# Kernel optimization log

Hardware: AMD Instinct MI355X
Metric: run time of the kernel (lower is better)

## Reference

```python
import jax, jax.numpy as jnp
import numpy as np


def setup_inputs() -> dict:
    key = jax.random.key(0)
    B, S, D, H = 4, 2048, 1024, 16
    hd = D // H
    ks = jax.random.split(key, 11)
    sc = 1.0 / np.sqrt(D)
    return {
        "keys": jax.random.normal(ks[0], (B, S, D), jnp.float32),
        "queries": jax.random.normal(ks[1], (B, S, D), jnp.float32),
        "values": jax.random.normal(ks[2], (B, S, D), jnp.float32),
        "Wq": jax.random.normal(ks[3], (H, D, hd), jnp.float32) * sc,
        "bq": jax.random.normal(ks[4], (H, hd), jnp.float32) * 0.02,
        "Wk": jax.random.normal(ks[5], (H, D, hd), jnp.float32) * sc,
        "bk": jax.random.normal(ks[6], (H, hd), jnp.float32) * 0.02,
        "Wv": jax.random.normal(ks[7], (H, D, hd), jnp.float32) * sc,
        "bv": jax.random.normal(ks[8], (H, hd), jnp.float32) * 0.02,
        "Wo": jax.random.normal(ks[9], (D, D), jnp.float32) * sc,
        "bo": jax.random.normal(ks[10], (D,), jnp.float32) * 0.02,
    }


def reference(keys, queries, values, Wq, bq, Wk, bk, Wv, bv, Wo, bo):
    # Per-head linear projections: [B,S,D] x [H,D,hd] -> [B,H,S,hd]
    q = jnp.einsum("bsd,hde->bhse", queries, Wq) + bq[None, :, None, :]
    k = jnp.einsum("bsd,hde->bhse", keys, Wk) + bk[None, :, None, :]
    v = jnp.einsum("bsd,hde->bhse", values, Wv) + bv[None, :, None, :]

    hd = q.shape[-1]
    S = q.shape[2]
    scores = jnp.einsum("bhse,bhte->bhst", q, k) / jnp.sqrt(jnp.float32(hd))
    causal = jnp.tril(jnp.ones((S, S), dtype=bool))  # tril buffer
    scores = jnp.where(causal[None, None, :, :], scores, -jnp.inf)
    attn = jax.nn.softmax(scores, axis=-1)  # dropout p=0 (eval)

    o = jnp.einsum("bhst,bhte->bhse", attn, v)  # [B,H,S,hd]
    # concat heads -> [B,S,H*hd]
    o = o.transpose(0, 2, 1, 3).reshape(o.shape[0], S, -1)
    return o @ Wo + bo
```

## Files before the change

### kernel.cpp

```cpp
#include <hip/hip_runtime.h>
#include <stdint.h>

typedef unsigned short u16;
typedef __attribute__((ext_vector_type(4))) float f32x4;
typedef __attribute__((ext_vector_type(8))) short bfrag;

static __device__ __forceinline__ u16 f2bf(float f) {
  union { float f; uint32_t u; } v; v.f = f;
  return (u16)((v.u + 0x7fffu + ((v.u >> 16) & 1u)) >> 16);
}
static __device__ __forceinline__ uint32_t cvtpk(float lo, float hi) {
  uint32_t r;
  asm("v_cvt_pk_bf16_f32 %0, %1, %2" : "=v"(r) : "v"(lo), "v"(hi));
  return r;
}
static __device__ __forceinline__ uint32_t pk2bf(float lo, float hi) {
  union { float f; uint32_t u; } a, b; a.f = lo; b.f = hi;
  return __builtin_amdgcn_perm(b.u + 0x8000u, a.u + 0x8000u, 0x07060302u);
}
static __device__ __forceinline__ float fexp2(float x) {
  float r;
  asm("v_exp_f32 %0, %1" : "=v"(r) : "v"(x));
  return r;
}

#define GLOAD16(gp, lp)                                              \
  __builtin_amdgcn_global_load_lds(                                  \
      (const __attribute__((address_space(1))) uint32_t*)(gp),       \
      (__attribute__((address_space(3))) uint32_t*)(lp), 16, 0, 0)

__global__ __launch_bounds__(256) void pack_w_hde(const float* __restrict__ W,
                                                  u16* __restrict__ Wt) {
  __shared__ float tile[64][65];
  const int h = blockIdx.y, k0 = blockIdx.x * 64;
  const int tid = threadIdx.x;
#pragma unroll
  for (int j = 0; j < 4; ++j) {
    int idx = tid + j * 256;
    int rr = idx >> 4, c4 = (idx & 15) * 4;
    const float4 v = *(const float4*)(W + (size_t)h * 65536 + (size_t)(k0 + rr) * 64 + c4);
    tile[rr][c4 + 0] = v.x; tile[rr][c4 + 1] = v.y;
    tile[rr][c4 + 2] = v.z; tile[rr][c4 + 3] = v.w;
  }
  __syncthreads();
#pragma unroll
  for (int j = 0; j < 4; ++j) {
    int idx = tid + j * 256;
    int ee = idx >> 4, c4 = (idx & 15) * 4;
    uint2 u;
    u.x = f2bf(tile[c4 + 0][ee]) | ((uint32_t)f2bf(tile[c4 + 1][ee]) << 16);
    u.y = f2bf(tile[c4 + 2][ee]) | ((uint32_t)f2bf(tile[c4 + 3][ee]) << 16);
    *(uint2*)(Wt + (size_t)(h * 64 + ee) * 1024 + k0 + c4) = u;
  }
}

__global__ __launch_bounds__(256) void transpose_w(const float* __restrict__ W,
                                                   u16* __restrict__ Wt) {
  __shared__ float tile[64][65];
  const int k0 = blockIdx.x * 64, n0 = blockIdx.y * 64;
  const int tid = threadIdx.x;
#pragma unroll
  for (int j = 0; j < 4; ++j) {
    int idx = tid + j * 256;
    int rr = idx >> 4, c4 = (idx & 15) * 4;
    const float4 v = *(const float4*)(W + (size_t)(k0 + rr) * 1024 + n0 + c4);
    tile[rr][c4 + 0] = v.x; tile[rr][c4 + 1] = v.y;
    tile[rr][c4 + 2] = v.z; tile[rr][c4 + 3] = v.w;
  }
  __syncthreads();
#pragma unroll
  for (int j = 0; j < 4; ++j) {
    int idx = tid + j * 256;
    int ee = idx >> 4, c4 = (idx & 15) * 4;
    uint2 u;
    u.x = f2bf(tile[c4 + 0][ee]) | ((uint32_t)f2bf(tile[c4 + 1][ee]) << 16);
    u.y = f2bf(tile[c4 + 2][ee]) | ((uint32_t)f2bf(tile[c4 + 3][ee]) << 16);
    *(uint2*)(Wt + (size_t)(n0 + ee) * 1024 + k0 + c4) = u;
  }
}

__global__ __launch_bounds__(256) void gemm_qkv(
    const float* __restrict__ Aq, const float* __restrict__ Ak,
    const float* __restrict__ Avv, const u16* __restrict__ Bt,
    const float* __restrict__ bq, const float* __restrict__ bk,
    const float* __restrict__ bv,
    u16* __restrict__ Qb, u16* __restrict__ Kb, u16* __restrict__ Vt) {
  __shared__ u16 As[2][128 * 32];
  __shared__ u16 Bs[2][128 * 32];
  const int tid = threadIdx.x;
  const int n = blockIdx.x;
  const int xcd = n & 7, j = n >> 3;
  const int mb = xcd * 8 + (j & 7);
  const int nb = j >> 3;
  const int chunk = nb >> 3;
  const float* Af = (chunk == 0) ? Aq : (chunk == 1) ? Ak : Avv;
  const int wid = tid >> 6, lane = tid & 63;
  const int wr = wid >> 1, wc = wid & 1;
  const int g = lane >> 4, l15 = lane & 15;
  f32x4 acc[4][4] = {};

  const int bsrc = ((lane & 3) ^ ((lane >> 3) & 3)) * 8;
  const u16* Bg = Bt + (size_t)(nb * 128 + 2 * wid * 16 + (lane >> 2)) * 1024 + bsrc;
  const float* Ap = Af + (size_t)(mb * 128 + (tid >> 2)) * 1024 + (tid & 3) * 8;
  const int arow = tid >> 2;
  const int acs = (((tid & 3) ^ ((tid >> 3) & 3))) * 8;
  const int swzr = (l15 >> 1) & 3;

  float4 fa[2][2];
#pragma unroll
  for (int c = 0; c < 2; ++c) {
    fa[c][0] = *(const float4*)(Ap + (size_t)c * 64 * 1024);
    fa[c][1] = *(const float4*)(Ap + (size_t)c * 64 * 1024 + 4);
  }
#pragma unroll
  for (int c = 0; c < 2; ++c)
    GLOAD16(Bg + (size_t)c * 16 * 1024, &Bs[0][2 * wid * 512 + c * 512]);
#pragma unroll
  for (int c = 0; c < 2; ++c) {
    uint4 u;
    u.x = pk2bf(fa[c][0].x, fa[c][0].y); u.y = pk2bf(fa[c][0].z, fa[c][0].w);
    u.z = pk2bf(fa[c][1].x, fa[c][1].y); u.w = pk2bf(fa[c][1].z, fa[c][1].w);
    *(uint4*)&As[0][(arow + c * 64) * 32 + acs] = u;
  }
  __syncthreads();
  int cur = 0;
  for (int kk = 0; kk < 32; ++kk) {
    if (kk < 31) {
      const int kn = (kk + 1) * 32;
#pragma unroll
      for (int c = 0; c < 2; ++c) {
        fa[c][0] = *(const float4*)(Ap + (size_t)c * 64 * 1024 + kn);
        fa[c][1] = *(const float4*)(Ap + (size_t)c * 64 * 1024 + kn + 4);
      }
#pragma unroll
      for (int c = 0; c < 2; ++c)
        GLOAD16(Bg + (size_t)c * 16 * 1024 + kn, &Bs[cur ^ 1][2 * wid * 512 + c * 512]);
    }
    bfrag a[4], b[4];
#pragma unroll
    for (int m = 0; m < 4; ++m)
      a[m] = __builtin_bit_cast(bfrag,
          *(const uint4*)&As[cur][(wr * 64 + m * 16 + l15) * 32 + ((g ^ swzr)) * 8]);
#pragma unroll
    for (int nn = 0; nn < 4; ++nn)
      b[nn] = __builtin_bit_cast(bfrag,
          *(const uint4*)&Bs[cur][(wc * 64 + nn * 16 + l15) * 32 + ((g ^ swzr)) * 8]);
    __builtin_amdgcn_s_setprio(1);
#pragma unroll
    for (int m = 0; m < 4; ++m)
#pragma unroll
      for (int nn = 0; nn < 4; ++nn)
        acc[m][nn] = __builtin_amdgcn_mfma_f32_16x16x32_bf16(a[m], b[nn], acc[m][nn], 0, 0, 0);
    __builtin_amdgcn_s_setprio(0);
    if (kk < 31) {
#pragma unroll
      for (int c = 0; c < 2; ++c) {
        uint4 u;
        u.x = pk2bf(fa[c][0].x, fa[c][0].y); u.y = pk2bf(fa[c][0].z, fa[c][0].w);
        u.z = pk2bf(fa[c][1].x, fa[c][1].y); u.w = pk2bf(fa[c][1].z, fa[c][1].w);
        *(uint4*)&As[cur ^ 1][(arow + c * 64) * 32 + acs] = u;
      }
      __syncthreads();
      cur ^= 1;
    }
  }

  const int row0 = mb * 128 + wr * 64 + g * 4;
  const int cc0 = (nb & 7) * 128 + wc * 64 + l15;
  const float* bias = (chunk == 0) ? bq : (chunk == 1) ? bk : bv;
  const float qs = (chunk == 0) ? 0.125f * 1.44269504f : 1.0f;
#pragma unroll
  for (int m = 0; m < 4; ++m) {
#pragma unroll
    for (int nn = 0; nn < 4; ++nn) {
      const int row = row0 + m * 16;
      const int cc = cc0 + nn * 16;
      const float bcv = bias[cc];
      if (chunk < 2) {
        u16* dst = (chunk == 0) ? Qb : Kb;
#pragma unroll
        for (int r = 0; r < 4; ++r)
          dst[(size_t)(row + r) * 1024 + cc] = f2bf((acc[m][nn][r] + bcv) * qs);
      } else {
        u16 w[4];
#pragma unroll
        for (int r = 0; r < 4; ++r) w[r] = f2bf(acc[m][nn][r] + bcv);
        const size_t dst =
            ((size_t)((row >> 11) * 16 + (cc >> 6)) * 64 + (cc & 63)) * 2048 + (row & 2047);
        *(uint2*)(Vt + dst) = *(const uint2*)w;
      }
    }
  }
}

__global__ __launch_bounds__(256) void gemm_o(const u16* __restrict__ Abf,
                                              const u16* __restrict__ Bt,
                                              const float* __restrict__ bo,
                                              float* __restrict__ Of) {
  __shared__ u16 As[2][128 * 32];
  __shared__ u16 Bs[2][128 * 32];
  const int tid = threadIdx.x;
  const int n = blockIdx.x;
  const int xcd = n & 7, j = n >> 3;
  const int mb = xcd * 8 + (j & 7);
  const int nb = j >> 3;
  const int wid = tid >> 6, lane = tid & 63;
  const int wr = wid >> 1, wc = wid & 1;
  const int g = lane >> 4, l15 = lane & 15;
  f32x4 acc[4][4] = {};

  const int bsrc = ((lane & 3) ^ ((lane >> 3) & 3)) * 8;
  const int swzr = (l15 >> 1) & 3;
  const u16* Bg = Bt + (size_t)(nb * 128 + 2 * wid * 16 + (lane >> 2)) * 1024 + bsrc;
  const u16* Ag = Abf + (size_t)(mb * 128 + 2 * wid * 16 + (lane >> 2)) * 1024 + bsrc;

#pragma unroll
  for (int c = 0; c < 2; ++c) {
    GLOAD16(Ag + (size_t)c * 16 * 1024, &As[0][2 * wid * 512 + c * 512]);
    GLOAD16(Bg + (size_t)c * 16 * 1024, &Bs[0][2 * wid * 512 + c * 512]);
  }
  __syncthreads();
  int cur = 0;
  for (int kk = 0; kk < 32; ++kk) {
    if (kk < 31) {
      const int kn = (kk + 1) * 32;
#pragma unroll
      for (int c = 0; c < 2; ++c) {
        GLOAD16(Ag + (size_t)c * 16 * 1024 + kn, &As[cur ^ 1][2 * wid * 512 + c * 512]);
        GLOAD16(Bg + (size_t)c * 16 * 1024 + kn, &Bs[cur ^ 1][2 * wid * 512 + c * 512]);
      }
    }
    bfrag a[4], b[4];
#pragma unroll
    for (int m = 0; m < 4; ++m)
      a[m] = __builtin_bit_cast(bfrag,
          *(const uint4*)&As[cur][(wr * 64 + m * 16 + l15) * 32 + ((g ^ swzr)) * 8]);
#pragma unroll
    for (int nn = 0; nn < 4; ++nn)
      b[nn] = __builtin_bit_cast(bfrag,
          *(const uint4*)&Bs[cur][(wc * 64 + nn * 16 + l15) * 32 + ((g ^ swzr)) * 8]);
    __builtin_amdgcn_s_setprio(1);
#pragma unroll
    for (int m = 0; m < 4; ++m)
#pragma unroll
      for (int nn = 0; nn < 4; ++nn)
        acc[m][nn] = __builtin_amdgcn_mfma_f32_16x16x32_bf16(a[m], b[nn], acc[m][nn], 0, 0, 0);
    __builtin_amdgcn_s_setprio(0);
    if (kk < 31) { __syncthreads(); cur ^= 1; }
  }

  const int row0 = mb * 128 + wr * 64 + g * 4;
  const int col0 = nb * 128 + wc * 64 + l15;
#pragma unroll
  for (int m = 0; m < 4; ++m)
#pragma unroll
    for (int nn = 0; nn < 4; ++nn) {
      const int row = row0 + m * 16, col = col0 + nn * 16;
      const float bcv = bo[col];
#pragma unroll
      for (int r = 0; r < 4; ++r)
        Of[(size_t)(row + r) * 1024 + col] = acc[m][nn][r] + bcv;
    }
}

__global__ __launch_bounds__(512) void attn_fused(const u16* __restrict__ Qb,
                                                  const u16* __restrict__ Kb,
                                                  const u16* __restrict__ Vtg,
                                                  u16* __restrict__ Ob) {
  __shared__ u16 KV[2][2][4096];
  const int tid = threadIdx.x;
  const int wid = tid >> 6, lane = tid & 63;
  const int g = lane >> 4, l15 = lane & 15;
  const int n = blockIdx.x;
  const int half = n >> 8, idx = n & 255;
  const int xcd = idx & 7;
  const int bh = xcd * 8 + ((idx >> 3) & 7);
  const int grp = idx >> 6;
  const int u = half ? grp : (7 - grp);
  const int t = u * 8 + wid;
  const int b = bh >> 4, h = bh & 15;
  const size_t baserow = (size_t)b * 2048;
  const u16* Qg = Qb + baserow * 1024 + h * 64;
  const u16* Kg = Kb + baserow * 1024 + h * 64;
  const u16* Vg = Vtg + (size_t)bh * 64 * 2048;
  u16* Og = Ob + baserow * 1024 + h * 64;

  const int q0 = t * 32;
  const int qrow = q0 + l15;
  const int mysteps = (q0 >> 6) + 1;
  const int smax = 4 * u + 4;
  const float M2 = 6.0f;

  const int sr = tid >> 3;
  const int scc = (tid & 7) ^ (sr & 7);
  const u16* Kst = Kg + (size_t)sr * 1024 + scc * 8;
  const u16* Vst = Vg + (size_t)sr * 2048 + scc * 8;

  bfrag qa[2][2];
#pragma unroll
  for (int qf = 0; qf < 2; ++qf)
#pragma unroll
    for (int kh = 0; kh < 2; ++kh)
      qa[qf][kh] = __builtin_bit_cast(bfrag,
          *(const uint4*)(Qg + (size_t)(q0 + qf * 16 + l15) * 1024 + kh * 32 + g * 8));

  f32x4 accT[2][4] = {};
  float Ll[2] = {0.f, 0.f};

  const int s0lane = ((g & 1) << 5) | l15;
  const int s1lane = s0lane + 16;
  const bool ghi = (g >= 2);
  const int swz = l15 & 7;

  GLOAD16(Kst, &KV[0][0][wid * 512]);
  GLOAD16(Vst, &KV[0][1][wid * 512]);
  __syncthreads();

  for (int s = 0; s < smax; ++s) {
    const int cb = s & 1;
    if (s + 1 < smax) {
      const size_t kn = (size_t)(s + 1) << 6;
      GLOAD16(Kst + kn * 1024, &KV[cb ^ 1][0][wid * 512]);
      GLOAD16(Vst + kn, &KV[cb ^ 1][1][wid * 512]);
    }
    if (s < mysteps) {
      const int kv0 = s << 6;
      const bool diag = (s == mysteps - 1);
      const u16* KB = &KV[cb][0][0];
      const u16* VB = &KV[cb][1][0];

      bfrag kb[2][4];
#pragma unroll
      for (int tt = 0; tt < 4; ++tt)
#pragma unroll
        for (int kh = 0; kh < 2; ++kh)
          kb[kh][tt] = __builtin_bit_cast(bfrag,
              *(const uint4*)&KB[(tt * 16 + l15) * 64 + (((kh << 2) | g) ^ swz) * 8]);

      f32x4 sc[2][4];
      __builtin_amdgcn_s_setprio(1);
#pragma unroll
      for (int qf = 0; qf < 2; ++qf)
#pragma unroll
        for (int tt = 0; tt < 4; ++tt) {
          f32x4 z = {0.f, 0.f, 0.f, 0.f};
          z = __builtin_amdgcn_mfma_f32_16x16x32_bf16(kb[0][tt], qa[qf][0], z, 0, 0, 0);
          z = __builtin_amdgcn_mfma_f32_16x16x32_bf16(kb[1][tt], qa[qf][1], z, 0, 0, 0);
          sc[qf][tt] = z;
        }
      __builtin_amdgcn_s_setprio(0);

      bfrag vb[2][4];
#pragma unroll
      for (int et = 0; et < 4; ++et)
#pragma unroll
        for (int kcb = 0; kcb < 2; ++kcb)
          vb[kcb][et] = __builtin_bit_cast(bfrag,
              *(const uint4*)&VB[(et * 16 + l15) * 64 + (((kcb << 2) | g) ^ swz) * 8]);

#pragma unroll
      for (int qf = 0; qf < 2; ++qf) {
        if (diag) {
          const int qq = qrow + qf * 16;
#pragma unroll
          for (int tt = 0; tt < 4; ++tt) {
            const int kvb = kv0 + tt * 16 + g * 4;
#pragma unroll
            for (int r = 0; r < 4; ++r)
              sc[qf][tt][r] = (kvb + r <= qq) ? sc[qf][tt][r] : -100.0f;
          }
        }
        uint32_t pk[4][2];
        float ss = 0.f;
#pragma unroll
        for (int tt = 0; tt < 4; ++tt) {
          float p0 = fexp2(sc[qf][tt][0] - M2);
          float p1 = fexp2(sc[qf][tt][1] - M2);
          float p2 = fexp2(sc[qf][tt][2] - M2);
          float p3 = fexp2(sc[qf][tt][3] - M2);
          ss += (p0 + p1) + (p2 + p3);
          pk[tt][0] = cvtpk(p0, p1);
          pk[tt][1] = cvtpk(p2, p3);
        }
        Ll[qf] += ss;
        __builtin_amdgcn_s_setprio(1);
#pragma unroll
        for (int kcb = 0; kcb < 2; ++kcb) {
          const int lo = kcb * 2, hi = kcb * 2 + 1;
          const uint32_t a0 = __shfl(pk[lo][0], s0lane), b0 = __shfl(pk[hi][0], s0lane);
          const uint32_t a1 = __shfl(pk[lo][1], s0lane), b1 = __shfl(pk[hi][1], s0lane);
          const uint32_t a2 = __shfl(pk[lo][0], s1lane), b2 = __shfl(pk[hi][0], s1lane);
          const uint32_t a3 = __shfl(pk[lo][1], s1lane), b3 = __shfl(pk[hi][1], s1lane);
          uint4 uu;
          uu.x = ghi ? b0 : a0; uu.y = ghi ? b1 : a1;
          uu.z = ghi ? b2 : a2; uu.w = ghi ? b3 : a3;
          const bfrag pfrag = __builtin_bit_cast(bfrag, uu);
#pragma unroll
          for (int et = 0; et < 4; ++et)
            accT[qf][et] = __builtin_amdgcn_mfma_f32_16x16x32_bf16(vb[kcb][et], pfrag, accT[qf][et], 0, 0, 0);
        }
        __builtin_amdgcn_s_setprio(0);
      }
    }
    __syncthreads();
  }

#pragma unroll
  for (int qf = 0; qf < 2; ++qf) {
    float Ls = Ll[qf];
    Ls += __shfl_xor(Ls, 16);
    Ls += __shfl_xor(Ls, 32);
    const float inv = 1.f / Ls;
    u16* orow = Og + (size_t)(q0 + qf * 16 + l15) * 1024 + g * 4;
#pragma unroll
    for (int et = 0; et < 4; ++et) {
      uint2 w;
      w.x = cvtpk(accT[qf][et][0] * inv, accT[qf][et][1] * inv);
      w.y = cvtpk(accT[qf][et][2] * inv, accT[qf][et][3] * inv);
      *(uint2*)(orow + et * 16) = w;
    }
  }
}

extern "C" void kernel_launch(void* const* d_in, const int* in_sizes, int n_in,
                              void* d_out, int out_size, void* d_ws, size_t ws_size,
                              hipStream_t stream) {
  const float* keys    = (const float*)d_in[0];
  const float* queries = (const float*)d_in[1];
  const float* values  = (const float*)d_in[2];
  const float* Wq = (const float*)d_in[3];
  const float* bq = (const float*)d_in[4];
  const float* Wk = (const float*)d_in[5];
  const float* bk = (const float*)d_in[6];
  const float* Wv = (const float*)d_in[7];
  const float* bv = (const float*)d_in[8];
  const float* Wo = (const float*)d_in[9];
  const float* bo = (const float*)d_in[10];
  float* out = (float*)d_out;

  char* ws = (char*)d_ws;
  const size_t MB = 1u << 20;
  u16* Wqkvt = (u16*)(ws);
  u16* Wot   = (u16*)(ws + 6 * MB);
  u16* Qb    = (u16*)(ws + 8 * MB);
  u16* Kb    = (u16*)(ws + 24 * MB);
  u16* Vtg   = (u16*)(ws + 40 * MB);
  u16* Ob    = (u16*)(ws + 56 * MB);

  const dim3 pg(16, 16);
  pack_w_hde<<<pg, 256, 0, stream>>>(Wq, Wqkvt);
  pack_w_hde<<<pg, 256, 0, stream>>>(Wk, Wqkvt + (size_t)1024 * 1024);
  pack_w_hde<<<pg, 256, 0, stream>>>(Wv, Wqkvt + (size_t)2048 * 1024);
  transpose_w<<<pg, 256, 0, stream>>>(Wo, Wot);

  gemm_qkv<<<dim3(1536), 256, 0, stream>>>(queries, keys, values, Wqkvt,
                                           bq, bk, bv, Qb, Kb, Vtg);

  attn_fused<<<dim3(512), 512, 0, stream>>>(Qb, Kb, Vtg, Ob);

  gemm_o<<<dim3(512), 256, 0, stream>>>(Ob, Wot, bo, out);
}
```

Before: 187.8 us.

## Widen QKV GEMM tile to 128x256 with 512-thread blocks

The QKV projection GEMM now uses a 128x256 output tile per block with 8 waves (2x4) instead of 128x128 with 4 waves, and the grid shrinks from 1536 to 768 blocks. Each fp32 A tile, loaded and converted to bf16, is now reused across twice as many output columns. This halves redundant global reads and conversions of the large fp32 activations. In exchange it uses more LDS per block and gives fewer, larger blocks, which could reduce occupancy or tail balance.

```diff
diff --git a/kernel.cpp b/kernel.cpp
--- a/kernel.cpp
+++ b/kernel.cpp
@@ -79,62 +79,54 @@
   }
 }
 
-__global__ __launch_bounds__(256) void gemm_qkv(
+__global__ __launch_bounds__(512) void gemm_qkv(
     const float* __restrict__ Aq, const float* __restrict__ Ak,
     const float* __restrict__ Avv, const u16* __restrict__ Bt,
     const float* __restrict__ bq, const float* __restrict__ bk,
     const float* __restrict__ bv,
     u16* __restrict__ Qb, u16* __restrict__ Kb, u16* __restrict__ Vt) {
   __shared__ u16 As[2][128 * 32];
-  __shared__ u16 Bs[2][128 * 32];
+  __shared__ u16 Bs[2][256 * 32];
   const int tid = threadIdx.x;
   const int n = blockIdx.x;
   const int xcd = n & 7, j = n >> 3;
   const int mb = xcd * 8 + (j & 7);
-  const int nb = j >> 3;
-  const int chunk = nb >> 3;
+  const int nb2 = j >> 3;
+  const int chunk = nb2 >> 2;
   const float* Af = (chunk == 0) ? Aq : (chunk == 1) ? Ak : Avv;
   const int wid = tid >> 6, lane = tid & 63;
-  const int wr = wid >> 1, wc = wid & 1;
+  const int wr = wid >> 2, wc = wid & 3;
   const int g = lane >> 4, l15 = lane & 15;
   f32x4 acc[4][4] = {};
 
   const int bsrc = ((lane & 3) ^ ((lane >> 3) & 3)) * 8;
-  const u16* Bg = Bt + (size_t)(nb * 128 + 2 * wid * 16 + (lane >> 2)) * 1024 + bsrc;
+  const u16* Bg = Bt + (size_t)(nb2 * 256 + 2 * wid * 16 + (lane >> 2)) * 1024 + bsrc;
   const float* Ap = Af + (size_t)(mb * 128 + (tid >> 2)) * 1024 + (tid & 3) * 8;
   const int arow = tid >> 2;
   const int acs = (((tid & 3) ^ ((tid >> 3) & 3))) * 8;
   const int swzr = (l15 >> 1) & 3;
 
-  float4 fa[2][2];
-#pragma unroll
-  for (int c = 0; c < 2; ++c) {
-    fa[c][0] = *(const float4*)(Ap + (size_t)c * 64 * 1024);
-    fa[c][1] = *(const float4*)(Ap + (size_t)c * 64 * 1024 + 4);
-  }
+  float4 fa0 = *(const float4*)(Ap);
+  float4 fa1 = *(const float4*)(Ap + 4);
 #pragma unroll
   for (int c = 0; c < 2; ++c)
-    GLOAD16(Bg + (size_t)c * 16 * 1024, &Bs[0][2 * wid * 512 + c * 512]);
-#pragma unroll
-  for (int c = 0; c < 2; ++c) {
+    GLOAD16(Bg + (size_t)c * 16 * 1024, &Bs[0][(2 * wid + c) * 512]);
+  {
     uint4 u;
-    u.x = pk2bf(fa[c][0].x, fa[c][0].y); u.y = pk2bf(fa[c][0].z, fa[c][0].w);
-    u.z = pk2bf(fa[c][1].x, fa[c][1].y); u.w = pk2bf(fa[c][1].z, fa[c][1].w);
-    *(uint4*)&As[0][(arow + c * 64) * 32 + acs] = u;
+    u.x = pk2bf(fa0.x, fa0.y); u.y = pk2bf(fa0.z, fa0.w);
+    u.z = pk2bf(fa1.x, fa1.y); u.w = pk2bf(fa1.z, fa1.w);
+    *(uint4*)&As[0][arow * 32 + acs] = u;
   }
   __syncthreads();
   int cur = 0;
   for (int kk = 0; kk < 32; ++kk) {
     if (kk < 31) {
       const int kn = (kk + 1) * 32;
-#pragma unroll
-      for (int c = 0; c < 2; ++c) {
-        fa[c][0] = *(const float4*)(Ap + (size_t)c * 64 * 1024 + kn);
-        fa[c][1] = *(const float4*)(Ap + (size_t)c * 64 * 1024 + kn + 4);
-      }
+      fa0 = *(const float4*)(Ap + kn);
+      fa1 = *(const float4*)(Ap + kn + 4);
 #pragma unroll
       for (int c = 0; c < 2; ++c)
-        GLOAD16(Bg + (size_t)c * 16 * 1024 + kn, &Bs[cur ^ 1][2 * wid * 512 + c * 512]);
+        GLOAD16(Bg + (size_t)c * 16 * 1024 + kn, &Bs[cur ^ 1][(2 * wid + c) * 512]);
     }
     bfrag a[4], b[4];
 #pragma unroll
@@ -153,20 +145,17 @@
         acc[m][nn] = __builtin_amdgcn_mfma_f32_16x16x32_bf16(a[m], b[nn], acc[m][nn], 0, 0, 0);
     __builtin_amdgcn_s_setprio(0);
     if (kk < 31) {
-#pragma unroll
-      for (int c = 0; c < 2; ++c) {
-        uint4 u;
-        u.x = pk2bf(fa[c][0].x, fa[c][0].y); u.y = pk2bf(fa[c][0].z, fa[c][0].w);
-        u.z = pk2bf(fa[c][1].x, fa[c][1].y); u.w = pk2bf(fa[c][1].z, fa[c][1].w);
-        *(uint4*)&As[cur ^ 1][(arow + c * 64) * 32 + acs] = u;
-      }
+      uint4 u;
+      u.x = pk2bf(fa0.x, fa0.y); u.y = pk2bf(fa0.z, fa0.w);
+      u.z = pk2bf(fa1.x, fa1.y); u.w = pk2bf(fa1.z, fa1.w);
+      *(uint4*)&As[cur ^ 1][arow * 32 + acs] = u;
       __syncthreads();
       cur ^= 1;
     }
   }
 
   const int row0 = mb * 128 + wr * 64 + g * 4;
-  const int cc0 = (nb & 7) * 128 + wc * 64 + l15;
+  const int ccL = (nb2 & 3) * 256 + wc * 64 + l15;
   const float* bias = (chunk == 0) ? bq : (chunk == 1) ? bk : bv;
   const float qs = (chunk == 0) ? 0.125f * 1.44269504f : 1.0f;
 #pragma unroll
@@ -174,7 +163,7 @@
 #pragma unroll
     for (int nn = 0; nn < 4; ++nn) {
       const int row = row0 + m * 16;
-      const int cc = cc0 + nn * 16;
+      const int cc = ccL + nn * 16;
       const float bcv = bias[cc];
       if (chunk < 2) {
         u16* dst = (chunk == 0) ? Qb : Kb;
@@ -453,8 +442,8 @@
   pack_w_hde<<<pg, 256, 0, stream>>>(Wv, Wqkvt + (size_t)2048 * 1024);
   transpose_w<<<pg, 256, 0, stream>>>(Wo, Wot);
 
-  gemm_qkv<<<dim3(1536), 256, 0, stream>>>(queries, keys, values, Wqkvt,
-                                           bq, bk, bv, Qb, Kb, Vtg);
+  gemm_qkv<<<dim3(768), 512, 0, stream>>>(queries, keys, values, Wqkvt,
+                                          bq, bk, bv, Qb, Kb, Vtg);
 
   attn_fused<<<dim3(512), 512, 0, stream>>>(Qb, Kb, Vtg, Ob);
 
```

Result: no change. 185.3 us (-1.4%).
